# Optimization experiments

Measured on AMD Instinct MI355X. Metric: run time of the kernel, lower is better.

The kernel has to match this reference:

```python
import jax, jax.numpy as jnp
import numpy as np

N_NODES = 100000
N_EDGES = 1600000
D_IN, D_HID, D_OUT = 128, 64, 40


def glorot(key, shape):
    lim = float(np.sqrt(6.0 / (shape[0] + shape[1])))
    return jax.random.uniform(key, shape, jnp.float32, -lim, lim)


def gcn_layer(x, W, b, src, dst, d_inv):
    # PyG GCNConv: linear first, then sym-normalized aggregation with self-loops.
    h = x @ W  # [N, d_out]
    coef = (d_inv[src] * d_inv[dst])[:, None]       # [E, 1]
    msg = h[src] * coef                              # [E, d_out] gather
    agg = jax.ops.segment_sum(msg, dst, num_segments=N_NODES)  # scatter-add
    agg = agg + h * (d_inv * d_inv)[:, None]         # self-loop contribution
    return agg + b


def setup_inputs() -> dict:
    key = jax.random.key(0)
    ks = jax.random.split(key, 8)
    x = jax.random.normal(ks[0], (N_NODES, D_IN), jnp.float32)
    edge_index = jax.random.randint(ks[1], (2, N_EDGES), 0, N_NODES, jnp.int64)
    return {
        "x": x,
        "edge_index": edge_index,
        "W1": glorot(ks[2], (D_IN, D_HID)), "b1": jnp.zeros((D_HID,), jnp.float32),
        "W2": glorot(ks[3], (D_HID, D_HID)), "b2": jnp.zeros((D_HID,), jnp.float32),
        "W3": glorot(ks[4], (D_HID, D_OUT)), "b3": jnp.zeros((D_OUT,), jnp.float32),
    }


def reference(x, edge_index, W1, b1, W2, b2, W3, b3):
    src, dst = edge_index[0], edge_index[1]
    # degree with self-loops (each node gets +1)
    deg = jax.ops.segment_sum(jnp.ones((N_EDGES,), jnp.float32), dst,
                              num_segments=N_NODES) + 1.0
    d_inv = jax.lax.rsqrt(deg)
    h = jax.nn.relu(gcn_layer(x, W1, b1, src, dst, d_inv))
    h = jax.nn.relu(gcn_layer(h, W2, b2, src, dst, d_inv))
    return gcn_layer(h, W3, b3, src, dst, d_inv)
```

## Files before the change

kernel.cpp:

```cpp
#include <hip/hip_runtime.h>
#include <hip/hip_bf16.h>


constexpr int BLK = 256;
constexpr int SB2 = 9;
constexpr int EPB = 4096;
constexpr int BUCKCAP = 10240;

typedef __attribute__((ext_vector_type(8))) short bf16x8;
typedef __attribute__((ext_vector_type(4))) float f32x4;

__device__ inline unsigned short bf_rne(float f) {
    unsigned int u = __float_as_uint(f);
    unsigned int r = (u + 0x7fffu + ((u >> 16) & 1u)) >> 16;
    return (unsigned short)r;
}
__device__ inline unsigned int pk(unsigned short lo, unsigned short hi) {
    return (unsigned int)lo | ((unsigned int)hi << 16);
}

__global__ __launch_bounds__(256) void part_hist(
    const int* __restrict__ dst, int* __restrict__ bh, int E, int nblk, int NB2) {
    __shared__ int lh[256];
    int k = blockIdx.x, t = threadIdx.x;
    lh[t] = 0;
    __syncthreads();
    const int4* dp = (const int4*)(dst + k * EPB);
#pragma unroll
    for (int j = 0; j < EPB / 1024; ++j) {
        int idx = j * 256 + t;
        int e = k * EPB + idx * 4;
        if (e < E) {
            int4 d4 = dp[idx];
            atomicAdd(&lh[d4.x >> SB2], 1);
            atomicAdd(&lh[d4.y >> SB2], 1);
            atomicAdd(&lh[d4.z >> SB2], 1);
            atomicAdd(&lh[d4.w >> SB2], 1);
        }
    }
    __syncthreads();
    if (t < NB2) bh[t * nblk + k] = lh[t];
}

__global__ __launch_bounds__(256) void part_scan(
    int* __restrict__ bh, int* __restrict__ btot, int nblk) {
    __shared__ int sh[256];
    int b = blockIdx.x, t = threadIdx.x;
    int base = b * BUCKCAP;
    int v[4]; int s = 0;
#pragma unroll
    for (int j = 0; j < 4; ++j) {
        int idx = t * 4 + j;
        v[j] = (idx < nblk) ? bh[b * nblk + idx] : 0;
        s += v[j];
    }
    sh[t] = s;
    __syncthreads();
    for (int off = 1; off < 256; off <<= 1) {
        int x = (t >= off) ? sh[t - off] : 0;
        __syncthreads();
        sh[t] += x;
        __syncthreads();
    }
    int run = sh[t] - s;
    if (t == 255) btot[b] = (sh[255] < BUCKCAP) ? sh[255] : BUCKCAP;
#pragma unroll
    for (int j = 0; j < 4; ++j) {
        int idx = t * 4 + j;
        if (idx < nblk) bh[b * nblk + idx] = base + run;
        run += v[j];
    }
}

__global__ __launch_bounds__(256) void part_scatter(
    const int* __restrict__ src, const int* __restrict__ dst,
    const int* __restrict__ bh, unsigned int* __restrict__ buf,
    int E, int nblk, int NB2) {
    __shared__ int lbase[256];
    __shared__ int lcnt[256];
    int k = blockIdx.x, t = threadIdx.x;
    lcnt[t] = 0;
    if (t < NB2) lbase[t] = bh[t * nblk + k];
    __syncthreads();
    const int4* dp = (const int4*)(dst + k * EPB);
    const int4* sp = (const int4*)(src + k * EPB);
#pragma unroll
    for (int j = 0; j < EPB / 1024; ++j) {
        int idx = j * 256 + t;
        int e = k * EPB + idx * 4;
        if (e < E) {
            int4 d4 = dp[idx];
            int4 s4 = sp[idx];
            int d, bkt, p;
            d = d4.x; bkt = d >> SB2; p = lbase[bkt] + atomicAdd(&lcnt[bkt], 1);
            buf[p] = ((unsigned int)(d & 511) << 23) | (unsigned int)s4.x;
            d = d4.y; bkt = d >> SB2; p = lbase[bkt] + atomicAdd(&lcnt[bkt], 1);
            buf[p] = ((unsigned int)(d & 511) << 23) | (unsigned int)s4.y;
            d = d4.z; bkt = d >> SB2; p = lbase[bkt] + atomicAdd(&lcnt[bkt], 1);
            buf[p] = ((unsigned int)(d & 511) << 23) | (unsigned int)s4.z;
            d = d4.w; bkt = d >> SB2; p = lbase[bkt] + atomicAdd(&lcnt[bkt], 1);
            buf[p] = ((unsigned int)(d & 511) << 23) | (unsigned int)s4.w;
        }
    }
}

__global__ __launch_bounds__(256) void csr_finalize(
    const unsigned int* __restrict__ buf, const int* __restrict__ btot,
    int* __restrict__ rptr, int* __restrict__ rdeg, float* __restrict__ dinv,
    int* __restrict__ csr, int N) {
    __shared__ int hist[1 << SB2];
    __shared__ int excl[1 << SB2];
    __shared__ int ssc[256];
    int b = blockIdx.x, t = threadIdx.x;
    int nb0 = b << SB2;
    int nn = N - nb0; if (nn > (1 << SB2)) nn = 1 << SB2;
    int beg = b * BUCKCAP;
    int end = beg + btot[b];

    hist[t] = 0; hist[t + 256] = 0;
    __syncthreads();
    for (int i = beg + t; i < end; i += 256)
        atomicAdd(&hist[buf[i] >> 23], 1);
    __syncthreads();

    int a0 = hist[2 * t], a1 = hist[2 * t + 1];
    int s = a0 + a1;
    ssc[t] = s;
    __syncthreads();
    for (int off = 1; off < 256; off <<= 1) {
        int x = (t >= off) ? ssc[t - off] : 0;
        __syncthreads();
        ssc[t] += x;
        __syncthreads();
    }
    int run = ssc[t] - s;
    excl[2 * t] = run;
    excl[2 * t + 1] = run + a0;
    __syncthreads();

    for (int j = t; j < nn; j += 256) {
        rptr[nb0 + j] = beg + excl[j];
        rdeg[nb0 + j] = hist[j];
        dinv[nb0 + j] = rsqrtf((float)hist[j] + 1.0f);
    }
    __syncthreads();

    hist[t] = 0; hist[t + 256] = 0;
    __syncthreads();
    for (int i = beg + t; i < end; i += 256) {
        unsigned int w = buf[i];
        int local = w >> 23;
        int p = beg + excl[local] + atomicAdd(&hist[local], 1);
        csr[p] = (int)(w & 0x7fffffu);
    }
}

template<int K, int NOUT, int HSTRIDE, bool AFP32>
__global__ __launch_bounds__(256) void gemm_mfma(
    const void* __restrict__ Aptr, const float* __restrict__ W,
    const float* __restrict__ d_inv, unsigned short* __restrict__ hs, int M)
{
    __shared__ unsigned short Wt[64][K + 8];
    __shared__ float Cst[64][68];

    const int t = threadIdx.x;
    const int wave = t >> 6, lane = t & 63;
    const int m = lane & 15, kq = lane >> 4;

    for (int idx = t; idx < K * 64; idx += 256) {
        int k = idx >> 6, c = idx & 63;
        float wv = (c < NOUT) ? W[k * NOUT + c] : 0.0f;
        Wt[c][k] = bf_rne(wv);
    }
    __syncthreads();

    const int rb = blockIdx.x * 64;
    int arow = rb + wave * 16 + m;
    if (arow >= M) arow = M - 1;

    f32x4 acc[4] = {{0.f,0.f,0.f,0.f},{0.f,0.f,0.f,0.f},
                    {0.f,0.f,0.f,0.f},{0.f,0.f,0.f,0.f}};
    union Frag { bf16x8 v; unsigned short u[8]; };

#pragma unroll
    for (int kc = 0; kc < K / 32; ++kc) {
        const int kbase = kc * 32 + kq * 8;
        Frag a;
        if (AFP32) {
            const float* ap = (const float*)Aptr + (size_t)arow * K + kbase;
            float4 x0 = *(const float4*)ap;
            float4 x1 = *(const float4*)(ap + 4);
            a.u[0] = bf_rne(x0.x); a.u[1] = bf_rne(x0.y);
            a.u[2] = bf_rne(x0.z); a.u[3] = bf_rne(x0.w);
            a.u[4] = bf_rne(x1.x); a.u[5] = bf_rne(x1.y);
            a.u[6] = bf_rne(x1.z); a.u[7] = bf_rne(x1.w);
        } else {
            const unsigned short* ap = (const unsigned short*)Aptr + (size_t)arow * 64 + kbase;
            a.v = *(const bf16x8*)ap;
        }
#pragma unroll
        for (int ct = 0; ct < 4; ++ct) {
            Frag b;
            b.v = *(const bf16x8*)(&Wt[ct * 16 + m][kbase]);
            acc[ct] = __builtin_amdgcn_mfma_f32_16x16x32_bf16(a.v, b.v, acc[ct], 0, 0, 0);
        }
    }

#pragma unroll
    for (int ct = 0; ct < 4; ++ct)
#pragma unroll
        for (int r = 0; r < 4; ++r)
            Cst[wave * 16 + kq * 4 + r][ct * 16 + m] = acc[ct][r];
    __syncthreads();

    int row = t >> 2, seg = t & 3;
    int grow = rb + row;
    int c0 = seg * 16;
    if (grow < M && c0 < NOUT) {
        float di = d_inv[grow];
        unsigned int uu[8];
#pragma unroll
        for (int j = 0; j < 8; ++j) {
            float v0 = Cst[row][c0 + 2 * j]     * di;
            float v1 = Cst[row][c0 + 2 * j + 1] * di;
            uu[j] = pk(bf_rne(v0), bf_rne(v1));
        }
        unsigned short* orow = hs + (size_t)grow * HSTRIDE + c0;
        *(uint4*)orow = make_uint4(uu[0], uu[1], uu[2], uu[3]);
        if (NOUT - c0 > 8)
            *((uint4*)orow + 1) = make_uint4(uu[4], uu[5], uu[6], uu[7]);
    }
}

template<int DACT, int HSTRIDE, bool RELU, bool OBF16, int OSTRIDE>
__global__ __launch_bounds__(256) void agg4(
    const unsigned short* __restrict__ hs, const int* __restrict__ rptr,
    const int* __restrict__ rdeg, const int* __restrict__ csr,
    const float* __restrict__ dinv, const float* __restrict__ b,
    void* __restrict__ out, int N)
{
    int i = (blockIdx.x * 256 + threadIdx.x) >> 4;
    if (i >= N) return;
    int lane = threadIdx.x & 63;
    int q  = lane & 15;
    int sb = lane & 48;
    constexpr int QACT = DACT / 4;
    const bool act = (q < QACT);

    int beg = rptr[i];
    int end = beg + rdeg[i];

    float a0 = 0.f, a1 = 0.f, a2 = 0.f, a3 = 0.f;
    float di = 0.f;
    float4 bv = make_float4(0.f, 0.f, 0.f, 0.f);
    if (act) {
        di = dinv[i];
        bv = *(const float4*)(b + q * 4);
        uint2 u0 = *(const uint2*)(hs + (size_t)i * HSTRIDE + q * 4);
        a0 = __uint_as_float(u0.x << 16);
        a1 = __uint_as_float(u0.x & 0xffff0000u);
        a2 = __uint_as_float(u0.y << 16);
        a3 = __uint_as_float(u0.y & 0xffff0000u);
    }

    for (int c = beg; c < end; c += 16) {
        int s_l = (c + q < end) ? csr[c + q] : 0;
        int m = end - c; if (m > 16) m = 16;
        int k = 0;
        for (; k + 8 <= m; k += 8) {
            int ss[8];
#pragma unroll
            for (int j = 0; j < 8; ++j) ss[j] = __shfl(s_l, sb | (k + j), 64);
            if (act) {
                uint2 vv[8];
#pragma unroll
                for (int j = 0; j < 8; ++j)
                    vv[j] = *(const uint2*)(hs + (size_t)ss[j] * HSTRIDE + q * 4);
#pragma unroll
                for (int j = 0; j < 8; ++j) {
                    a0 += __uint_as_float(vv[j].x << 16);
                    a1 += __uint_as_float(vv[j].x & 0xffff0000u);
                    a2 += __uint_as_float(vv[j].y << 16);
                    a3 += __uint_as_float(vv[j].y & 0xffff0000u);
                }
            }
        }
        for (; k < m; ++k) {
            int s = __shfl(s_l, sb | k, 64);
            if (act) {
                uint2 u = *(const uint2*)(hs + (size_t)s * HSTRIDE + q * 4);
                a0 += __uint_as_float(u.x << 16);
                a1 += __uint_as_float(u.x & 0xffff0000u);
                a2 += __uint_as_float(u.y << 16);
                a3 += __uint_as_float(u.y & 0xffff0000u);
            }
        }
    }

    if (act) {
        a0 = di * a0 + bv.x; a1 = di * a1 + bv.y;
        a2 = di * a2 + bv.z; a3 = di * a3 + bv.w;
        if (RELU) {
            a0 = fmaxf(a0, 0.f); a1 = fmaxf(a1, 0.f);
            a2 = fmaxf(a2, 0.f); a3 = fmaxf(a3, 0.f);
        }
        if (OBF16) {
            unsigned short* ob = (unsigned short*)out;
            uint2 o;
            o.x = pk(bf_rne(a0), bf_rne(a1));
            o.y = pk(bf_rne(a2), bf_rne(a3));
            *(uint2*)(ob + (size_t)i * 64 + q * 4) = o;
        } else {
            float* of = (float*)out;
            *(float4*)(of + (size_t)i * OSTRIDE + q * 4) = make_float4(a0, a1, a2, a3);
        }
    }
}

extern "C" void kernel_launch(void* const* d_in, const int* in_sizes, int n_in,
                              void* d_out, int out_size, void* d_ws, size_t ws_size,
                              hipStream_t stream) {
    const float* x   = (const float*)d_in[0];
    const int*   ei  = (const int*)  d_in[1];
    const float* W1  = (const float*)d_in[2];
    const float* bb1 = (const float*)d_in[3];
    const float* W2  = (const float*)d_in[4];
    const float* bb2 = (const float*)d_in[5];
    const float* W3  = (const float*)d_in[6];
    const float* bb3 = (const float*)d_in[7];
    float* out = (float*)d_out;

    const int N = in_sizes[0] / 128;
    const int E = in_sizes[1] / 2;
    const int* src = ei;
    const int* dst = ei + E;
    const int NB2  = (N + (1 << SB2) - 1) >> SB2;
    const int nblk = (E + EPB - 1) / EPB;

    float* ws = (float*)d_ws;
    const size_t NP  = ((size_t)N + 255) & ~255ull;
    float* dinv = ws;
    unsigned short* bufHs  = (unsigned short*)(ws + NP);
    unsigned short* bufAct = bufHs + (size_t)N * 64;
    int*   rptr  = (int*)(bufAct + (size_t)N * 64);
    int*   rdeg  = rptr + N;
    int*   btot  = rdeg + N;
    int*   bh    = btot + 256;
    size_t bhsz  = ((size_t)NB2 * nblk + 1) & ~1ull;
    unsigned int* buf = (unsigned int*)(bh + bhsz);
    int*   csr   = (int*)(buf + (size_t)NB2 * BUCKCAP);
    int*   bar   = csr + (size_t)NB2 * BUCKCAP;
    (void)bar;

    dim3 blk(BLK);
    int gRows = (N + 63) / 64;
    int gQW   = (N * 16 + BLK - 1) / BLK;

    part_hist<<<nblk, blk, 0, stream>>>(dst, bh, E, nblk, NB2);
    part_scan<<<NB2, blk, 0, stream>>>(bh, btot, nblk);
    part_scatter<<<nblk, blk, 0, stream>>>(src, dst, bh, buf, E, nblk, NB2);
    csr_finalize<<<NB2, blk, 0, stream>>>(buf, btot, rptr, rdeg, dinv, csr, N);

    gemm_mfma<128, 64, 64, true><<<gRows, blk, 0, stream>>>(x, W1, dinv, bufHs, N);
    agg4<64, 64, true, true, 64><<<gQW, blk, 0, stream>>>(bufHs, rptr, rdeg, csr, dinv, bb1, bufAct, N);

    gemm_mfma<64, 64, 64, false><<<gRows, blk, 0, stream>>>(bufAct, W2, dinv, bufHs, N);
    agg4<64, 64, true, true, 64><<<gQW, blk, 0, stream>>>(bufHs, rptr, rdeg, csr, dinv, bb2, bufAct, N);

    gemm_mfma<64, 40, 40, false><<<gRows, blk, 0, stream>>>(bufAct, W3, dinv, bufHs, N);
    agg4<40, 40, false, false, 40><<<gQW, blk, 0, stream>>>(bufHs, rptr, rdeg, csr, dinv, bb3, out, N);
}
```

Measured before the change: 284.1 us.

## Fuse partition histogram, scan and scatter into one kernel with global atomics

The three-kernel edge partitioning (per-block histogram, per-bucket scan, scatter) becomes a single kernel. Each block builds its local bucket histogram, claims a contiguous range in each bucket with a global atomicAdd on the bucket totals, then scatters its edges. The dst values are kept in registers between the two phases. This removes two kernel launches, the block-histogram array traffic and a second read of dst, at the cost of a memset and a nondeterministic edge order inside each bucket, which can change floating-point summation order.

```diff
diff --git a/kernel.cpp b/kernel.cpp
--- a/kernel.cpp
+++ b/kernel.cpp
@@ -19,87 +19,58 @@
     return (unsigned int)lo | ((unsigned int)hi << 16);
 }
 
-__global__ __launch_bounds__(256) void part_hist(
-    const int* __restrict__ dst, int* __restrict__ bh, int E, int nblk, int NB2) {
-    __shared__ int lh[256];
-    int k = blockIdx.x, t = threadIdx.x;
-    lh[t] = 0;
-    __syncthreads();
+__global__ __launch_bounds__(256) void part_fused(
+    const int* __restrict__ src, const int* __restrict__ dst,
+    int* __restrict__ btot, unsigned int* __restrict__ buf,
+    int E, int NB2)
+{
+    __shared__ int lcnt[256];
+    __shared__ int lbase[256];
+    const int k = blockIdx.x, t = threadIdx.x;
+    lcnt[t] = 0;
+    __syncthreads();
+
+    int4 d[4];
+    bool val[4];
     const int4* dp = (const int4*)(dst + k * EPB);
 #pragma unroll
-    for (int j = 0; j < EPB / 1024; ++j) {
+    for (int j = 0; j < 4; ++j) {
         int idx = j * 256 + t;
         int e = k * EPB + idx * 4;
-        if (e < E) {
-            int4 d4 = dp[idx];
-            atomicAdd(&lh[d4.x >> SB2], 1);
-            atomicAdd(&lh[d4.y >> SB2], 1);
-            atomicAdd(&lh[d4.z >> SB2], 1);
-            atomicAdd(&lh[d4.w >> SB2], 1);
-        }
-    }
-    __syncthreads();
-    if (t < NB2) bh[t * nblk + k] = lh[t];
-}
-
-__global__ __launch_bounds__(256) void part_scan(
-    int* __restrict__ bh, int* __restrict__ btot, int nblk) {
-    __shared__ int sh[256];
-    int b = blockIdx.x, t = threadIdx.x;
-    int base = b * BUCKCAP;
-    int v[4]; int s = 0;
+        val[j] = (e < E);
+        if (val[j]) {
+            d[j] = dp[idx];
+            atomicAdd(&lcnt[d[j].x >> SB2], 1);
+            atomicAdd(&lcnt[d[j].y >> SB2], 1);
+            atomicAdd(&lcnt[d[j].z >> SB2], 1);
+            atomicAdd(&lcnt[d[j].w >> SB2], 1);
+        }
+    }
+    __syncthreads();
+
+    if (t < NB2) {
+        int c = lcnt[t];
+        lbase[t] = t * BUCKCAP + atomicAdd(&btot[t], c);
+    }
+    __syncthreads();
+    lcnt[t] = 0;
+    __syncthreads();
+
+    const int4* sp = (const int4*)(src + k * EPB);
 #pragma unroll
     for (int j = 0; j < 4; ++j) {
-        int idx = t * 4 + j;
-        v[j] = (idx < nblk) ? bh[b * nblk + idx] : 0;
-        s += v[j];
-    }
-    sh[t] = s;
-    __syncthreads();
-    for (int off = 1; off < 256; off <<= 1) {
-        int x = (t >= off) ? sh[t - off] : 0;
-        __syncthreads();
-        sh[t] += x;
-        __syncthreads();
-    }
-    int run = sh[t] - s;
-    if (t == 255) btot[b] = (sh[255] < BUCKCAP) ? sh[255] : BUCKCAP;
-#pragma unroll
-    for (int j = 0; j < 4; ++j) {
-        int idx = t * 4 + j;
-        if (idx < nblk) bh[b * nblk + idx] = base + run;
-        run += v[j];
-    }
-}
-
-__global__ __launch_bounds__(256) void part_scatter(
-    const int* __restrict__ src, const int* __restrict__ dst,
-    const int* __restrict__ bh, unsigned int* __restrict__ buf,
-    int E, int nblk, int NB2) {
-    __shared__ int lbase[256];
-    __shared__ int lcnt[256];
-    int k = blockIdx.x, t = threadIdx.x;
-    lcnt[t] = 0;
-    if (t < NB2) lbase[t] = bh[t * nblk + k];
-    __syncthreads();
-    const int4* dp = (const int4*)(dst + k * EPB);
-    const int4* sp = (const int4*)(src + k * EPB);
-#pragma unroll
-    for (int j = 0; j < EPB / 1024; ++j) {
         int idx = j * 256 + t;
-        int e = k * EPB + idx * 4;
-        if (e < E) {
-            int4 d4 = dp[idx];
+        if (val[j]) {
             int4 s4 = sp[idx];
-            int d, bkt, p;
-            d = d4.x; bkt = d >> SB2; p = lbase[bkt] + atomicAdd(&lcnt[bkt], 1);
-            buf[p] = ((unsigned int)(d & 511) << 23) | (unsigned int)s4.x;
-            d = d4.y; bkt = d >> SB2; p = lbase[bkt] + atomicAdd(&lcnt[bkt], 1);
-            buf[p] = ((unsigned int)(d & 511) << 23) | (unsigned int)s4.y;
-            d = d4.z; bkt = d >> SB2; p = lbase[bkt] + atomicAdd(&lcnt[bkt], 1);
-            buf[p] = ((unsigned int)(d & 511) << 23) | (unsigned int)s4.z;
-            d = d4.w; bkt = d >> SB2; p = lbase[bkt] + atomicAdd(&lcnt[bkt], 1);
-            buf[p] = ((unsigned int)(d & 511) << 23) | (unsigned int)s4.w;
+            int dd, bkt, p;
+            dd = d[j].x; bkt = dd >> SB2; p = lbase[bkt] + atomicAdd(&lcnt[bkt], 1);
+            buf[p] = ((unsigned int)(dd & 511) << 23) | (unsigned int)s4.x;
+            dd = d[j].y; bkt = dd >> SB2; p = lbase[bkt] + atomicAdd(&lcnt[bkt], 1);
+            buf[p] = ((unsigned int)(dd & 511) << 23) | (unsigned int)s4.y;
+            dd = d[j].z; bkt = dd >> SB2; p = lbase[bkt] + atomicAdd(&lcnt[bkt], 1);
+            buf[p] = ((unsigned int)(dd & 511) << 23) | (unsigned int)s4.z;
+            dd = d[j].w; bkt = dd >> SB2; p = lbase[bkt] + atomicAdd(&lcnt[bkt], 1);
+            buf[p] = ((unsigned int)(dd & 511) << 23) | (unsigned int)s4.w;
         }
     }
 }
@@ -115,7 +86,8 @@
     int nb0 = b << SB2;
     int nn = N - nb0; if (nn > (1 << SB2)) nn = 1 << SB2;
     int beg = b * BUCKCAP;
-    int end = beg + btot[b];
+    int tot = btot[b]; if (tot > BUCKCAP) tot = BUCKCAP;
+    int end = beg + tot;
 
     hist[t] = 0; hist[t + 256] = 0;
     __syncthreads();
@@ -349,16 +321,13 @@
     size_t bhsz  = ((size_t)NB2 * nblk + 1) & ~1ull;
     unsigned int* buf = (unsigned int*)(bh + bhsz);
     int*   csr   = (int*)(buf + (size_t)NB2 * BUCKCAP);
-    int*   bar   = csr + (size_t)NB2 * BUCKCAP;
-    (void)bar;
 
     dim3 blk(BLK);
     int gRows = (N + 63) / 64;
     int gQW   = (N * 16 + BLK - 1) / BLK;
 
-    part_hist<<<nblk, blk, 0, stream>>>(dst, bh, E, nblk, NB2);
-    part_scan<<<NB2, blk, 0, stream>>>(bh, btot, nblk);
-    part_scatter<<<nblk, blk, 0, stream>>>(src, dst, bh, buf, E, nblk, NB2);
+    hipMemsetAsync(btot, 0, NB2 * sizeof(int), stream);
+    part_fused<<<nblk, blk, 0, stream>>>(src, dst, btot, buf, E, NB2);
     csr_finalize<<<NB2, blk, 0, stream>>>(buf, btot, rptr, rdeg, dinv, csr, N);
 
     gemm_mfma<128, 64, 64, true><<<gRows, blk, 0, stream>>>(x, W1, dinv, bufHs, N);
```

Measured after the change: 288.4 us. About the same (+1.5%).
